# Performance work log

Measured on AMD Instinct MI355X. Metric: run time of the kernel, lower is better.

The kernel has to match this reference:

```python
import jax, jax.numpy as jnp
import numpy as np

B, GL, GF, N = 4, 4, 128, 1024
CS, CN, NA = 32, 16, 16
S, HS = 512, 512


def squash(s, axis):
    # mag_sq/(1+mag_sq) * s/mag == s * mag/(1+mag_sq)
    mag_sq = jnp.sum(s * s, axis=axis, keepdims=True)
    return s * (jnp.sqrt(mag_sq) / (1.0 + mag_sq))


def routing(u_hat, n_iter=3):
    # u_hat: [M, I, J, U]; dynamic routing, softmax over J, squash over J (as in source)
    M, I, J, U = u_hat.shape
    b = jnp.zeros((I, J), dtype=u_hat.dtype)
    v = None
    for _ in range(n_iter):
        c = jax.nn.softmax(b, axis=1)                       # [I, J]
        s = jnp.einsum('ij,miju->mju', c, u_hat)            # [M, J, U]
        v = squash(s, axis=1)                               # squash over J (torch dim=2)
        b = b + jnp.einsum('miju,mju->mij', u_hat, v).mean(axis=0)
    return v


def setup_inputs():
    key = jax.random.key(0)
    ks = jax.random.split(key, 7)
    sc = 0.1
    return {
        'graph_embed': jax.random.normal(ks[0], (B, GL, GF, N), jnp.float32),
        'hidden': jax.random.normal(ks[1], (B, S, HS), jnp.float32),
        'Wp': jax.random.normal(ks[2], (GL, CS, GL, GF), jnp.float32) * sc,  # per-unit conv kernels
        'bp': jax.random.normal(ks[3], (GL, CS), jnp.float32) * sc,
        'Wg': jax.random.normal(ks[4], (CS, CN, CS, GL), jnp.float32) * sc,  # graph caps [I,J,U,K]
        'Wa': jax.random.normal(ks[5], (CS + HS,), jnp.float32) * sc,        # attention_1 weight
        'Ws': jax.random.normal(ks[6], (CN, NA, CS, CS), jnp.float32) * sc,  # aspect caps [I,J,U,K]
    }


def _per_example(x, h, Wp, bp, Wg, Wa, Ws):
    # x: [GL, GF, N], h: [S, HS]
    gl, gf, n = x.shape
    # primary capsules: each unit's conv kernel covers all (GL,GF) -> full contraction
    u = jnp.einsum('uclf,lfn->ucn', Wp, x) + bp[:, :, None]   # [GL, CS, N]
    u = squash(u.reshape(gl, -1), axis=1)                     # squash over CS*N (torch dim=2)
    p = u.reshape(n, gl, CS)                                  # torch .view(-1, GL, CS)
    # graph capsule routing
    u_hat_g = jnp.einsum('ijuk,mik->miju', Wg, p.transpose(0, 2, 1))  # [N, CS, CN, CS]
    v_g = routing(u_hat_g)                                    # [N, CN, CS]
    g = v_g.reshape(n, CS, CN).mean(axis=0).reshape(CN, CS)   # torch .view semantics
    # adaptive attention: Linear([g;h]) with no bias, softmax over capsules
    score = jax.nn.softmax((g @ Wa[:CS])[None, :] + (h @ Wa[CS:])[:, None], axis=1)  # [S, CN]
    condensed = g[None, :, :] * score[:, :, None]             # [S, CN, CS]
    # aspect capsule routing (transpose(1,2) then layer-internal transpose cancel out)
    u_hat_a = jnp.einsum('ijuk,mik->miju', Ws, condensed)     # [S, CN, NA, CS]
    return routing(u_hat_a)                                   # [S, NA, CS]


def reference(graph_embed, hidden, Wp, bp, Wg, Wa, Ws):
    f = jax.vmap(_per_example, in_axes=(0, 0, None, None, None, None, None))
    return f(graph_embed, hidden, Wp, bp, Wg, Wa, Ws)   # [B, S, NA, CS]
```

## Files before the change

kernel.cpp:

```cpp
#include <hip/hip_runtime.h>
#include <math.h>


static constexpr int OFF_U  = 0;
static constexpr int OFF_S  = 524288;
static constexpr int OFF_SS = 2621440;
static constexpr int OFF_BG = 2621456;
static constexpr int OFF_G  = 2623504;
static constexpr int OFF_VA = 2625552;
static constexpr int OFF_MS = 2627600;
static constexpr int OFF_UH = 2758672;

__global__ void k_primary_part(const float* __restrict__ X, const float* __restrict__ Wp,
                               float* __restrict__ Upart)
{
    __shared__ float Wt[128 * 68];
    const int ct = blockIdx.x, nt = blockIdx.y;
    const int b = blockIdx.z >> 2, ks = blockIdx.z & 3;
    const int t = threadIdx.x;
    const int tn = t & 15, tc = t >> 4;
    const int c0 = ct * 64, n0 = nt * 64;
#pragma unroll
    for (int i = 0; i < 8; ++i) {
        const int idx = t + i * 256;
        const int c = idx >> 5, k4 = idx & 31;
        const float4 wv = *(const float4*)&Wp[(size_t)(c0 + c) * 512 + ks * 128 + k4 * 4];
        Wt[(k4 * 4 + 0) * 68 + c] = wv.x;
        Wt[(k4 * 4 + 1) * 68 + c] = wv.y;
        Wt[(k4 * 4 + 2) * 68 + c] = wv.z;
        Wt[(k4 * 4 + 3) * 68 + c] = wv.w;
    }
    __syncthreads();
    float acc[4][4] = {};
    const float* Xp = X + (size_t)b * 524288 + (size_t)(ks * 128) * 1024 + n0 + tn * 4;
#pragma unroll 4
    for (int k = 0; k < 128; ++k) {
        const float4 xv = *(const float4*)(Xp + (size_t)k * 1024);
        const float4 wv = *(const float4*)&Wt[k * 68 + tc * 4];
        const float w[4] = {wv.x, wv.y, wv.z, wv.w};
        const float x[4] = {xv.x, xv.y, xv.z, xv.w};
#pragma unroll
        for (int ci = 0; ci < 4; ++ci)
#pragma unroll
            for (int ni = 0; ni < 4; ++ni)
                acc[ci][ni] = fmaf(w[ci], x[ni], acc[ci][ni]);
    }
    float* up = Upart + (size_t)ks * 524288 + (size_t)b * 131072;
#pragma unroll
    for (int ci = 0; ci < 4; ++ci)
        *(float4*)&up[(size_t)(c0 + tc * 4 + ci) * 1024 + n0 + tn * 4] =
            make_float4(acc[ci][0], acc[ci][1], acc[ci][2], acc[ci][3]);
}

__global__ void k_reduceU(const float* __restrict__ Upart, const float* __restrict__ bp,
                          float* __restrict__ U, float* __restrict__ SS)
{
    __shared__ float red[256];
    const int blk = blockIdx.x, t = threadIdx.x;
    const int b = blk >> 5, cg = blk & 31;
    float ssq = 0.f;
#pragma unroll
    for (int i = 0; i < 4; ++i) {
        const int c = cg * 4 + i;
        const int f4 = b * 32768 + c * 256 + t;
        float4 s = ((const float4*)Upart)[f4];
#pragma unroll
        for (int ks = 1; ks < 4; ++ks) {
            const float4 p = ((const float4*)Upart)[ks * 131072 + f4];
            s.x += p.x; s.y += p.y; s.z += p.z; s.w += p.w;
        }
        const float bv = bp[c];
        s.x += bv; s.y += bv; s.z += bv; s.w += bv;
        ssq = fmaf(s.x, s.x, ssq); ssq = fmaf(s.y, s.y, ssq);
        ssq = fmaf(s.z, s.z, ssq); ssq = fmaf(s.w, s.w, ssq);
        ((float4*)U)[f4] = s;
    }
    red[t] = ssq;
    __syncthreads();
    for (int s = 128; s > 0; s >>= 1) {
        if (t < s) red[t] += red[t + s];
        __syncthreads();
    }
    if (t == 0) atomicAdd(&SS[b * 4 + (cg >> 3)], red[0]);
}

__global__ void k_smatmul(const float* __restrict__ U, const float* __restrict__ SS,
                          const float* __restrict__ Bg, const float* __restrict__ Wg,
                          float* __restrict__ S)
{
    __shared__ float Pt[64 * 65];
    __shared__ float Ct[64 * 65];
    __shared__ float cls[512];
    const int mt = blockIdx.x, jt = blockIdx.y, b = blockIdx.z;
    const int t = threadIdx.x;
    const int tj = t & 15, tm = t >> 4;
    if (t < 32) {
        float vals[16];
        float mx = -1e30f;
        for (int j = 0; j < 16; ++j) { vals[j] = Bg[b * 512 + t * 16 + j]; mx = fmaxf(mx, vals[j]); }
        float sum = 0.f;
        for (int j = 0; j < 16; ++j) { vals[j] = expf(vals[j] - mx); sum += vals[j]; }
        const float inv = 1.f / sum;
        for (int j = 0; j < 16; ++j) cls[t * 16 + j] = vals[j] * inv;
    }
    const float ss = SS[b * 4 + (mt >> 2)];
    const float sc = sqrtf(ss) / (1.f + ss);
    float acc[4][4] = {};
    const float* Ub = U + (size_t)b * 131072 + (size_t)mt * 64 * 128;
    __syncthreads();
    for (int kc = 0; kc < 2; ++kc) {
        for (int x = t; x < 64 * 64; x += 256) {
            const int r = x >> 6, cq = x & 63;
            Pt[r * 65 + cq] = Ub[r * 128 + kc * 64 + cq] * sc;
            const int q = kc * 64 + cq;
            const int i = q & 31, kk = q >> 5;
            const int ju = jt * 64 + r;
            const int j = ju >> 5, u = ju & 31;
            Ct[r * 65 + cq] = cls[i * 16 + j] * Wg[((i * 16 + j) * 32 + u) * 4 + kk];
        }
        __syncthreads();
        for (int q = 0; q < 64; ++q) {
            float pv[4], cv[4];
#pragma unroll
            for (int mm = 0; mm < 4; ++mm) pv[mm] = Pt[(tm * 4 + mm) * 65 + q];
#pragma unroll
            for (int jj = 0; jj < 4; ++jj) cv[jj] = Ct[(tj * 4 + jj) * 65 + q];
#pragma unroll
            for (int mm = 0; mm < 4; ++mm)
#pragma unroll
                for (int jj = 0; jj < 4; ++jj)
                    acc[mm][jj] = fmaf(pv[mm], cv[jj], acc[mm][jj]);
        }
        __syncthreads();
    }
#pragma unroll
    for (int mm = 0; mm < 4; ++mm) {
        float4 w = make_float4(acc[mm][0], acc[mm][1], acc[mm][2], acc[mm][3]);
        *(float4*)(S + (size_t)b * 524288 + (size_t)(mt * 64 + tm * 4 + mm) * 512
                     + jt * 64 + tj * 4) = w;
    }
}

__global__ void k_mag(const float* __restrict__ S, float* __restrict__ MS)
{
    const int t = threadIdx.x;
    const int u = t & 31, ml = t >> 5;
    const int m = blockIdx.x * 8 + ml;
    const int b = blockIdx.y;
    const float* row = S + (size_t)b * 524288 + (size_t)m * 512;
    float mag = 0.f;
#pragma unroll
    for (int j = 0; j < 16; ++j) { const float v = row[j * 32 + u]; mag = fmaf(v, v, mag); }
    MS[b * 32768 + m * 32 + u] = sqrtf(mag) / (1.f + mag);
}

__global__ void k_maggmean(const float* __restrict__ S, float* __restrict__ G)
{
    __shared__ float gacc[512];
    const int t = threadIdx.x;
    gacc[t] = 0.f; gacc[t + 256] = 0.f;
    const int u = t & 31, mlg = t >> 5;
    const int b = blockIdx.y;
    const int m0 = blockIdx.x * 32 + mlg * 4;
    float preg[16];
#pragma unroll
    for (int j = 0; j < 16; ++j) preg[j] = 0.f;
    __syncthreads();
#pragma unroll
    for (int mi = 0; mi < 4; ++mi) {
        const float* row = S + (size_t)b * 524288 + (size_t)(m0 + mi) * 512;
        float sv[16];
        float mag = 0.f;
#pragma unroll
        for (int j = 0; j < 16; ++j) { sv[j] = row[j * 32 + u]; mag = fmaf(sv[j], sv[j], mag); }
        const float msc = sqrtf(mag) / (1.f + mag);
#pragma unroll
        for (int j = 0; j < 16; ++j) preg[j] = fmaf(sv[j], msc, preg[j]);
    }
#pragma unroll
    for (int j = 0; j < 16; ++j) atomicAdd(&gacc[j * 32 + u], preg[j]);
    __syncthreads();
    atomicAdd(&G[b * 512 + t], gacc[t] * (1.f / 1024.f));
    atomicAdd(&G[b * 512 + 256 + t], gacc[t + 256] * (1.f / 1024.f));
}

__global__ void k_tbu(const float* __restrict__ U, const float* __restrict__ SS,
                      const float* __restrict__ S, const float* __restrict__ MS,
                      const float* __restrict__ Wg, float* __restrict__ Bg)
{
    __shared__ float Ps[64 * 132];
    __shared__ float Vs[64 * 68];
    __shared__ float bup[64];
    const int jt = blockIdx.x, mc = blockIdx.y, b = blockIdx.z;
    const int t = threadIdx.x;
    const int tq = t & 31, tjv = t >> 5;
    const int m0 = mc * 64;
    if (t < 64) bup[t] = 0.f;
    const float ss = SS[b * 4 + (mc >> 2)];
    const float sc = sqrtf(ss) / (1.f + ss);
#pragma unroll
    for (int i = 0; i < 8; ++i) {
        const int f4 = t + i * 256;
        const int r = f4 >> 5, q4 = f4 & 31;
        float4 v = *(const float4*)&U[(size_t)b * 131072 + (size_t)(m0 + r) * 128 + q4 * 4];
        v.x *= sc; v.y *= sc; v.z *= sc; v.w *= sc;
        *(float4*)&Ps[r * 132 + q4 * 4] = v;
    }
#pragma unroll
    for (int i = 0; i < 4; ++i) {
        const int f4 = t + i * 256;
        const int r = f4 >> 4, c4 = f4 & 15;
        const int m = m0 + r;
        float4 v = *(const float4*)&S[(size_t)b * 524288 + (size_t)m * 512 + jt * 64 + c4 * 4];
        const int ub = (c4 * 4) & 31;
        const float* msp = MS + b * 32768 + m * 32;
        v.x *= msp[ub + 0]; v.y *= msp[ub + 1]; v.z *= msp[ub + 2]; v.w *= msp[ub + 3];
        *(float4*)&Vs[r * 68 + c4 * 4] = v;
    }
    __syncthreads();
    float acc[4][8] = {};
#pragma unroll 2
    for (int m = 0; m < 64; ++m) {
        const float4 p4 = *(const float4*)&Ps[m * 132 + tq * 4];
        const float4 va = *(const float4*)&Vs[m * 68 + tjv * 8];
        const float4 vb = *(const float4*)&Vs[m * 68 + tjv * 8 + 4];
        const float pv[4] = {p4.x, p4.y, p4.z, p4.w};
        const float vv[8] = {va.x, va.y, va.z, va.w, vb.x, vb.y, vb.z, vb.w};
#pragma unroll
        for (int qi = 0; qi < 4; ++qi)
#pragma unroll
            for (int ji = 0; ji < 8; ++ji)
                acc[qi][ji] = fmaf(pv[qi], vv[ji], acc[qi][ji]);
    }
    const int k = tq >> 3;
    const int j_loc = tjv >> 2;
    const int j = jt * 2 + j_loc;
    const int u0 = (tjv & 3) * 8;
#pragma unroll
    for (int qi = 0; qi < 4; ++qi) {
        const int i = (tq & 7) * 4 + qi;
        const float* wp = Wg + ((i * 16 + j) * 32) * 4 + k;
        float s = 0.f;
#pragma unroll
        for (int ji = 0; ji < 8; ++ji)
            s = fmaf(wp[(u0 + ji) * 4], acc[qi][ji], s);
        s += __shfl_xor(s, 8);
        s += __shfl_xor(s, 16);
        s += __shfl_xor(s, 32);
        if ((t & 56) == 0) atomicAdd(&bup[i * 2 + j_loc], s);
    }
    __syncthreads();
    if (t < 64) {
        const int ii = t >> 1, jl = t & 1;
        atomicAdd(&Bg[b * 512 + ii * 16 + jt * 2 + jl], bup[t] * (1.f / 1024.f));
    }
}

__global__ void k_uhat(const float* __restrict__ G, const float* __restrict__ Wa,
                       const float* __restrict__ Ws, float* __restrict__ UH)
{
    const int b = blockIdx.y;
    const int t = threadIdx.x;
    __shared__ float g[512], cond[512], score[16], red[16];
    g[t] = G[b * 512 + t];
    g[t + 256] = G[b * 512 + 256 + t];
    __syncthreads();
    if (t < 16) {
        float s = 0.f;
        for (int u = 0; u < 32; ++u) s = fmaf(g[t * 32 + u], Wa[u], s);
        red[t] = s;
    }
    __syncthreads();
    if (t == 0) {
        float mx = -1e30f;
        for (int j = 0; j < 16; ++j) mx = fmaxf(mx, red[j]);
        float sum = 0.f;
        for (int j = 0; j < 16; ++j) { score[j] = expf(red[j] - mx); sum += score[j]; }
        const float inv = 1.f / sum;
        for (int j = 0; j < 16; ++j) score[j] *= inv;
    }
    __syncthreads();
    cond[t] = g[t] * score[t >> 5];
    cond[t + 256] = g[t + 256] * score[(t + 256) >> 5];
    __syncthreads();
    const int e0 = blockIdx.x * 1024 + t * 4;
    const int i = e0 >> 9;
    const float* cp = cond + i * 32;
    const float* wp = Ws + (size_t)e0 * 32;
    float res[4];
#pragma unroll
    for (int jj = 0; jj < 4; ++jj) {
        float s = 0.f;
#pragma unroll
        for (int k8 = 0; k8 < 8; ++k8) {
            const float4 w = *(const float4*)(wp + jj * 32 + k8 * 4);
            s = fmaf(w.x, cp[k8 * 4 + 0], s);
            s = fmaf(w.y, cp[k8 * 4 + 1], s);
            s = fmaf(w.z, cp[k8 * 4 + 2], s);
            s = fmaf(w.w, cp[k8 * 4 + 3], s);
        }
        res[jj] = s;
    }
    ((float4*)UH)[(b * 8192 + e0) >> 2] = make_float4(res[0], res[1], res[2], res[3]);
}

__global__ void k_route(const float* __restrict__ UH, float* __restrict__ VA)
{
    const int b = blockIdx.x;
    const int t = threadIdx.x;
    __shared__ float uh[8192], ba[256], cc[256], sbuf[512], msc[32];
#pragma unroll
    for (int i = 0; i < 8; ++i)
        ((float4*)uh)[i * 256 + t] = ((const float4*)UH)[b * 2048 + i * 256 + t];
    ba[t] = 0.f;
    __syncthreads();
    for (int it = 0; it < 3; ++it) {
        if (t < 16) {
            float mx = -1e30f;
            for (int j = 0; j < 16; ++j) mx = fmaxf(mx, ba[t * 16 + j]);
            float sum = 0.f;
            for (int j = 0; j < 16; ++j) { cc[t * 16 + j] = expf(ba[t * 16 + j] - mx); sum += cc[t * 16 + j]; }
            const float inv = 1.f / sum;
            for (int j = 0; j < 16; ++j) cc[t * 16 + j] *= inv;
        }
        __syncthreads();
        for (int h = 0; h < 2; ++h) {
            const int e = h * 256 + t;
            const int j = e >> 5;
            float s = 0.f;
            for (int i = 0; i < 16; ++i) s = fmaf(cc[i * 16 + j], uh[i * 512 + e], s);
            sbuf[e] = s;
        }
        __syncthreads();
        if (t < 32) {
            float mg = 0.f;
            for (int j = 0; j < 16; ++j) { const float x = sbuf[j * 32 + t]; mg = fmaf(x, x, mg); }
            msc[t] = sqrtf(mg) / (1.f + mg);
        }
        __syncthreads();
        for (int h = 0; h < 2; ++h) {
            const int e = h * 256 + t;
            sbuf[e] *= msc[e & 31];
        }
        __syncthreads();
        if (it < 2) {
            const int i = t >> 4, j = t & 15;
            float s = 0.f;
            for (int u = 0; u < 32; ++u) s = fmaf(uh[i * 512 + j * 32 + u], sbuf[j * 32 + u], s);
            ba[t] += s;
            __syncthreads();
        }
    }
    VA[b * 512 + t] = sbuf[t];
    VA[b * 512 + 256 + t] = sbuf[256 + t];
}

__global__ void k_out(const float* __restrict__ VA, float* __restrict__ out)
{
    const int idx = blockIdx.x * 256 + threadIdx.x;
    const int b = idx >> 16;
    const int jv4 = idx & 127;
    ((float4*)out)[idx] = ((const float4*)VA)[b * 128 + jv4];
}

extern "C" void kernel_launch(void* const* d_in, const int* in_sizes, int n_in,
                              void* d_out, int out_size, void* d_ws, size_t ws_size,
                              hipStream_t stream)
{
    const float* X   = (const float*)d_in[0];
    const float* Wp  = (const float*)d_in[2];
    const float* bp  = (const float*)d_in[3];
    const float* Wg  = (const float*)d_in[4];
    const float* Wa  = (const float*)d_in[5];
    const float* Wsp = (const float*)d_in[6];
    float* out = (float*)d_out;
    float* ws = (float*)d_ws;

    float* U  = ws + OFF_U;
    float* S  = ws + OFF_S;
    float* SS = ws + OFF_SS;
    float* Bg = ws + OFF_BG;
    float* G  = ws + OFF_G;
    float* VA = ws + OFF_VA;
    float* MS = ws + OFF_MS;
    float* UH = ws + OFF_UH;

    hipMemsetAsync(SS, 0, (16 + 2048 + 2048) * sizeof(float), stream);

    k_primary_part<<<dim3(2, 16, 16), 256, 0, stream>>>(X, Wp, S);
    k_reduceU<<<128, 256, 0, stream>>>(S, bp, U, SS);

    for (int it = 0; it < 3; ++it) {
        k_smatmul<<<dim3(16, 8, 4), 256, 0, stream>>>(U, SS, Bg, Wg, S);
        if (it < 2) {
            k_mag<<<dim3(128, 4), 256, 0, stream>>>(S, MS);
            k_tbu<<<dim3(8, 16, 4), 256, 0, stream>>>(U, SS, S, MS, Wg, Bg);
        } else {
            k_maggmean<<<dim3(32, 4), 256, 0, stream>>>(S, G);
        }
    }

    k_uhat<<<dim3(8, 4), 256, 0, stream>>>(G, Wa, Wsp, UH);
    k_route<<<4, 256, 0, stream>>>(UH, VA);
    k_out<<<1024, 256, 0, stream>>>(VA, out);
}
```

Measured before the change: 230.1 us.

## Fuse all stages into one persistent kernel with software grid barriers

Replaces the chain of about fourteen kernel launches and the memset with a single persistent kernel of 256 blocks that runs every stage in turn, separated by an atomic-counter grid barrier. Each stage's work is mapped onto the fixed block count with repeat loops. The aim is to remove launch gaps and per-kernel ramp-up and tail effects. In exchange, stages that used more blocks now run serially per block, many blocks sit idle in the small stages, and correctness depends on all 256 blocks being resident at once.

```diff
diff --git a/kernel.cpp b/kernel.cpp
--- a/kernel.cpp
+++ b/kernel.cpp
@@ -11,356 +11,412 @@
 static constexpr int OFF_MS = 2627600;
 static constexpr int OFF_UH = 2758672;
 
-__global__ void k_primary_part(const float* __restrict__ X, const float* __restrict__ Wp,
-                               float* __restrict__ Upart)
+#define NBLK 256
+
+__device__ unsigned g_cnt = 0;
+__device__ unsigned g_gen = 0;
+
+__device__ __forceinline__ void gbar()
 {
-    __shared__ float Wt[128 * 68];
-    const int ct = blockIdx.x, nt = blockIdx.y;
-    const int b = blockIdx.z >> 2, ks = blockIdx.z & 3;
+    __syncthreads();
+    if (threadIdx.x == 0) {
+        __threadfence();
+        const unsigned gen = atomicAdd(&g_gen, 0u);
+        if (atomicAdd(&g_cnt, 1u) == NBLK - 1u) {
+            atomicExch(&g_cnt, 0u);
+            __threadfence();
+            atomicAdd(&g_gen, 1u);
+        } else {
+            while (atomicAdd(&g_gen, 0u) == gen) { __builtin_amdgcn_s_sleep(8); }
+        }
+        __threadfence();
+    }
+    __syncthreads();
+}
+
+__global__ void __launch_bounds__(256, 1) k_mega(
+    const float* __restrict__ X,  const float* __restrict__ Wp,
+    const float* __restrict__ bp, const float* __restrict__ Wg,
+    const float* __restrict__ Wa, const float* __restrict__ Wsp,
+    float* __restrict__ ws, float* __restrict__ out)
+{
+    __shared__ float smem[12864];
+    const int bid = blockIdx.x;
     const int t = threadIdx.x;
-    const int tn = t & 15, tc = t >> 4;
-    const int c0 = ct * 64, n0 = nt * 64;
-#pragma unroll
-    for (int i = 0; i < 8; ++i) {
-        const int idx = t + i * 256;
-        const int c = idx >> 5, k4 = idx & 31;
-        const float4 wv = *(const float4*)&Wp[(size_t)(c0 + c) * 512 + ks * 128 + k4 * 4];
-        Wt[(k4 * 4 + 0) * 68 + c] = wv.x;
-        Wt[(k4 * 4 + 1) * 68 + c] = wv.y;
-        Wt[(k4 * 4 + 2) * 68 + c] = wv.z;
-        Wt[(k4 * 4 + 3) * 68 + c] = wv.w;
-    }
-    __syncthreads();
-    float acc[4][4] = {};
-    const float* Xp = X + (size_t)b * 524288 + (size_t)(ks * 128) * 1024 + n0 + tn * 4;
+
+    float* U  = ws + OFF_U;
+    float* S  = ws + OFF_S;
+    float* SS = ws + OFF_SS;
+    float* Bg = ws + OFF_BG;
+    float* G  = ws + OFF_G;
+    float* VA = ws + OFF_VA;
+    float* MS = ws + OFF_MS;
+    float* UH = ws + OFF_UH;
+
+    if (bid == 0) {
+        for (int i = t; i < 4112; i += 256) SS[i] = 0.f;
+    }
+
+    {
+        float* Wt = smem;
+        for (int rep = 0; rep < 2; ++rep) {
+            const int u = bid + rep * 256;
+            const int ct = u & 1, nt = (u >> 1) & 15;
+            const int z = u >> 5, b = z >> 2, ks = z & 3;
+            const int tn = t & 15, tc = t >> 4;
+            const int c0 = ct * 64, n0 = nt * 64;
+            __syncthreads();
+#pragma unroll
+            for (int i = 0; i < 8; ++i) {
+                const int idx = t + i * 256;
+                const int c = idx >> 5, k4 = idx & 31;
+                const float4 wv = *(const float4*)&Wp[(size_t)(c0 + c) * 512 + ks * 128 + k4 * 4];
+                Wt[(k4 * 4 + 0) * 68 + c] = wv.x;
+                Wt[(k4 * 4 + 1) * 68 + c] = wv.y;
+                Wt[(k4 * 4 + 2) * 68 + c] = wv.z;
+                Wt[(k4 * 4 + 3) * 68 + c] = wv.w;
+            }
+            __syncthreads();
+            float acc[4][4] = {};
+            const float* Xp = X + (size_t)b * 524288 + (size_t)(ks * 128) * 1024 + n0 + tn * 4;
 #pragma unroll 4
-    for (int k = 0; k < 128; ++k) {
-        const float4 xv = *(const float4*)(Xp + (size_t)k * 1024);
-        const float4 wv = *(const float4*)&Wt[k * 68 + tc * 4];
-        const float w[4] = {wv.x, wv.y, wv.z, wv.w};
-        const float x[4] = {xv.x, xv.y, xv.z, xv.w};
-#pragma unroll
-        for (int ci = 0; ci < 4; ++ci)
-#pragma unroll
-            for (int ni = 0; ni < 4; ++ni)
-                acc[ci][ni] = fmaf(w[ci], x[ni], acc[ci][ni]);
-    }
-    float* up = Upart + (size_t)ks * 524288 + (size_t)b * 131072;
-#pragma unroll
-    for (int ci = 0; ci < 4; ++ci)
-        *(float4*)&up[(size_t)(c0 + tc * 4 + ci) * 1024 + n0 + tn * 4] =
-            make_float4(acc[ci][0], acc[ci][1], acc[ci][2], acc[ci][3]);
-}
-
-__global__ void k_reduceU(const float* __restrict__ Upart, const float* __restrict__ bp,
-                          float* __restrict__ U, float* __restrict__ SS)
-{
-    __shared__ float red[256];
-    const int blk = blockIdx.x, t = threadIdx.x;
-    const int b = blk >> 5, cg = blk & 31;
-    float ssq = 0.f;
+            for (int k = 0; k < 128; ++k) {
+                const float4 xv = *(const float4*)(Xp + (size_t)k * 1024);
+                const float4 wv = *(const float4*)&Wt[k * 68 + tc * 4];
+                const float w[4] = {wv.x, wv.y, wv.z, wv.w};
+                const float x[4] = {xv.x, xv.y, xv.z, xv.w};
+#pragma unroll
+                for (int ci = 0; ci < 4; ++ci)
+#pragma unroll
+                    for (int ni = 0; ni < 4; ++ni)
+                        acc[ci][ni] = fmaf(w[ci], x[ni], acc[ci][ni]);
+            }
+            float* up = S + (size_t)ks * 524288 + (size_t)b * 131072;
+#pragma unroll
+            for (int ci = 0; ci < 4; ++ci)
+                *(float4*)&up[(size_t)(c0 + tc * 4 + ci) * 1024 + n0 + tn * 4] =
+                    make_float4(acc[ci][0], acc[ci][1], acc[ci][2], acc[ci][3]);
+        }
+    }
+    gbar();
+
+    if (bid < 128) {
+        float* red = smem;
+        const int b = bid >> 5, cg = bid & 31;
+        float ssq = 0.f;
+#pragma unroll
+        for (int i = 0; i < 4; ++i) {
+            const int c = cg * 4 + i;
+            const int f4 = b * 32768 + c * 256 + t;
+            float4 s = ((const float4*)S)[f4];
+#pragma unroll
+            for (int ks = 1; ks < 4; ++ks) {
+                const float4 p = ((const float4*)S)[ks * 131072 + f4];
+                s.x += p.x; s.y += p.y; s.z += p.z; s.w += p.w;
+            }
+            const float bv = bp[c];
+            s.x += bv; s.y += bv; s.z += bv; s.w += bv;
+            ssq = fmaf(s.x, s.x, ssq); ssq = fmaf(s.y, s.y, ssq);
+            ssq = fmaf(s.z, s.z, ssq); ssq = fmaf(s.w, s.w, ssq);
+            ((float4*)U)[f4] = s;
+        }
+        red[t] = ssq;
+        __syncthreads();
+        for (int s = 128; s > 0; s >>= 1) {
+            if (t < s) red[t] += red[t + s];
+            __syncthreads();
+        }
+        if (t == 0) atomicAdd(&SS[b * 4 + (cg >> 3)], red[0]);
+    }
+    gbar();
+
+    for (int it = 0; it < 3; ++it) {
+        {
+            float* Pt  = smem;
+            float* Ct  = smem + 4160;
+            float* cls = smem + 8320;
+            for (int rep = 0; rep < 2; ++rep) {
+                const int u = bid + rep * 256;
+                const int mt = u & 15, jt = (u >> 4) & 7, b = u >> 7;
+                const int tj = t & 15, tm = t >> 4;
+                __syncthreads();
+                if (t < 32) {
+                    float vals[16];
+                    float mx = -1e30f;
+                    for (int j = 0; j < 16; ++j) { vals[j] = Bg[b * 512 + t * 16 + j]; mx = fmaxf(mx, vals[j]); }
+                    float sum = 0.f;
+                    for (int j = 0; j < 16; ++j) { vals[j] = expf(vals[j] - mx); sum += vals[j]; }
+                    const float inv = 1.f / sum;
+                    for (int j = 0; j < 16; ++j) cls[t * 16 + j] = vals[j] * inv;
+                }
+                const float ssv = SS[b * 4 + (mt >> 2)];
+                const float sc = sqrtf(ssv) / (1.f + ssv);
+                float acc[4][4] = {};
+                const float* Ub = U + (size_t)b * 131072 + (size_t)mt * 64 * 128;
+                __syncthreads();
+                for (int kc = 0; kc < 2; ++kc) {
+                    for (int x = t; x < 64 * 64; x += 256) {
+                        const int r = x >> 6, cq = x & 63;
+                        Pt[r * 65 + cq] = Ub[r * 128 + kc * 64 + cq] * sc;
+                        const int q = kc * 64 + cq;
+                        const int i = q & 31, kk = q >> 5;
+                        const int ju = jt * 64 + r;
+                        const int j = ju >> 5, uu = ju & 31;
+                        Ct[r * 65 + cq] = cls[i * 16 + j] * Wg[((i * 16 + j) * 32 + uu) * 4 + kk];
+                    }
+                    __syncthreads();
+                    for (int q = 0; q < 64; ++q) {
+                        float pv[4], cv[4];
+#pragma unroll
+                        for (int mm = 0; mm < 4; ++mm) pv[mm] = Pt[(tm * 4 + mm) * 65 + q];
+#pragma unroll
+                        for (int jj = 0; jj < 4; ++jj) cv[jj] = Ct[(tj * 4 + jj) * 65 + q];
+#pragma unroll
+                        for (int mm = 0; mm < 4; ++mm)
+#pragma unroll
+                            for (int jj = 0; jj < 4; ++jj)
+                                acc[mm][jj] = fmaf(pv[mm], cv[jj], acc[mm][jj]);
+                    }
+                    __syncthreads();
+                }
+#pragma unroll
+                for (int mm = 0; mm < 4; ++mm) {
+                    float4 w = make_float4(acc[mm][0], acc[mm][1], acc[mm][2], acc[mm][3]);
+                    *(float4*)(S + (size_t)b * 524288 + (size_t)(mt * 64 + tm * 4 + mm) * 512
+                                 + jt * 64 + tj * 4) = w;
+                }
+            }
+        }
+        gbar();
+
+        if (it < 2) {
+            for (int rep = 0; rep < 2; ++rep) {
+                const int u = bid + rep * 256;
+                const int b = u >> 7, mg = u & 127;
+                const int uu = t & 31, ml = t >> 5;
+                const int m = mg * 8 + ml;
+                const float* row = S + (size_t)b * 524288 + (size_t)m * 512;
+                float mag = 0.f;
+#pragma unroll
+                for (int j = 0; j < 16; ++j) { const float v = row[j * 32 + uu]; mag = fmaf(v, v, mag); }
+                MS[b * 32768 + m * 32 + uu] = sqrtf(mag) / (1.f + mag);
+            }
+            gbar();
+
+            {
+                float* Ps  = smem;
+                float* Vs  = smem + 8448;
+                float* bup = smem + 12800;
+                for (int rep = 0; rep < 2; ++rep) {
+                    const int u = bid + rep * 256;
+                    const int jt = u & 7, mc = (u >> 3) & 15, b = u >> 7;
+                    const int tq = t & 31, tjv = t >> 5;
+                    const int m0 = mc * 64;
+                    __syncthreads();
+                    if (t < 64) bup[t] = 0.f;
+                    const float ssv = SS[b * 4 + (mc >> 2)];
+                    const float sc = sqrtf(ssv) / (1.f + ssv);
+#pragma unroll
+                    for (int i = 0; i < 8; ++i) {
+                        const int f4 = t + i * 256;
+                        const int r = f4 >> 5, q4 = f4 & 31;
+                        float4 v = *(const float4*)&U[(size_t)b * 131072 + (size_t)(m0 + r) * 128 + q4 * 4];
+                        v.x *= sc; v.y *= sc; v.z *= sc; v.w *= sc;
+                        *(float4*)&Ps[r * 132 + q4 * 4] = v;
+                    }
+#pragma unroll
+                    for (int i = 0; i < 4; ++i) {
+                        const int f4 = t + i * 256;
+                        const int r = f4 >> 4, c4 = f4 & 15;
+                        const int m = m0 + r;
+                        float4 v = *(const float4*)&S[(size_t)b * 524288 + (size_t)m * 512 + jt * 64 + c4 * 4];
+                        const int ub = (c4 * 4) & 31;
+                        const float* msp = MS + b * 32768 + m * 32;
+                        v.x *= msp[ub + 0]; v.y *= msp[ub + 1]; v.z *= msp[ub + 2]; v.w *= msp[ub + 3];
+                        *(float4*)&Vs[r * 68 + c4 * 4] = v;
+                    }
+                    __syncthreads();
+                    float acc[4][8] = {};
+#pragma unroll 2
+                    for (int m = 0; m < 64; ++m) {
+                        const float4 p4 = *(const float4*)&Ps[m * 132 + tq * 4];
+                        const float4 va = *(const float4*)&Vs[m * 68 + tjv * 8];
+                        const float4 vb = *(const float4*)&Vs[m * 68 + tjv * 8 + 4];
+                        const float pv[4] = {p4.x, p4.y, p4.z, p4.w};
+                        const float vv[8] = {va.x, va.y, va.z, va.w, vb.x, vb.y, vb.z, vb.w};
+#pragma unroll
+                        for (int qi = 0; qi < 4; ++qi)
+#pragma unroll
+                            for (int ji = 0; ji < 8; ++ji)
+                                acc[qi][ji] = fmaf(pv[qi], vv[ji], acc[qi][ji]);
+                    }
+                    const int k = tq >> 3;
+                    const int j_loc = tjv >> 2;
+                    const int j = jt * 2 + j_loc;
+                    const int u0 = (tjv & 3) * 8;
+#pragma unroll
+                    for (int qi = 0; qi < 4; ++qi) {
+                        const int i = (tq & 7) * 4 + qi;
+                        const float* wp = Wg + ((i * 16 + j) * 32) * 4 + k;
+                        float s = 0.f;
+#pragma unroll
+                        for (int ji = 0; ji < 8; ++ji)
+                            s = fmaf(wp[(u0 + ji) * 4], acc[qi][ji], s);
+                        s += __shfl_xor(s, 8);
+                        s += __shfl_xor(s, 16);
+                        s += __shfl_xor(s, 32);
+                        if ((t & 56) == 0) atomicAdd(&bup[i * 2 + j_loc], s);
+                    }
+                    __syncthreads();
+                    if (t < 64) {
+                        const int ii = t >> 1, jl = t & 1;
+                        atomicAdd(&Bg[b * 512 + ii * 16 + jt * 2 + jl], bup[t] * (1.f / 1024.f));
+                    }
+                }
+            }
+            gbar();
+        } else {
+            if (bid < 128) {
+                float* gacc = smem;
+                const int mt = bid & 31, b = bid >> 5;
+                gacc[t] = 0.f; gacc[t + 256] = 0.f;
+                const int uu = t & 31, mlg = t >> 5;
+                const int m0 = mt * 32 + mlg * 4;
+                float preg[16];
+#pragma unroll
+                for (int j = 0; j < 16; ++j) preg[j] = 0.f;
+                __syncthreads();
+#pragma unroll
+                for (int mi = 0; mi < 4; ++mi) {
+                    const float* row = S + (size_t)b * 524288 + (size_t)(m0 + mi) * 512;
+                    float sv[16];
+                    float mag = 0.f;
+#pragma unroll
+                    for (int j = 0; j < 16; ++j) { sv[j] = row[j * 32 + uu]; mag = fmaf(sv[j], sv[j], mag); }
+                    const float msc = sqrtf(mag) / (1.f + mag);
+#pragma unroll
+                    for (int j = 0; j < 16; ++j) preg[j] = fmaf(sv[j], msc, preg[j]);
+                }
+#pragma unroll
+                for (int j = 0; j < 16; ++j) atomicAdd(&gacc[j * 32 + uu], preg[j]);
+                __syncthreads();
+                atomicAdd(&G[b * 512 + t], gacc[t] * (1.f / 1024.f));
+                atomicAdd(&G[b * 512 + 256 + t], gacc[t + 256] * (1.f / 1024.f));
+            }
+            gbar();
+        }
+    }
+
+    if (bid < 32) {
+        float* g     = smem;
+        float* cond  = smem + 512;
+        float* score = smem + 1024;
+        float* red   = smem + 1040;
+        const int slice = bid & 7, b = bid >> 3;
+        g[t] = G[b * 512 + t];
+        g[t + 256] = G[b * 512 + 256 + t];
+        __syncthreads();
+        if (t < 16) {
+            float s = 0.f;
+            for (int uu = 0; uu < 32; ++uu) s = fmaf(g[t * 32 + uu], Wa[uu], s);
+            red[t] = s;
+        }
+        __syncthreads();
+        if (t == 0) {
+            float mx = -1e30f;
+            for (int j = 0; j < 16; ++j) mx = fmaxf(mx, red[j]);
+            float sum = 0.f;
+            for (int j = 0; j < 16; ++j) { score[j] = expf(red[j] - mx); sum += score[j]; }
+            const float inv = 1.f / sum;
+            for (int j = 0; j < 16; ++j) score[j] *= inv;
+        }
+        __syncthreads();
+        cond[t] = g[t] * score[t >> 5];
+        cond[t + 256] = g[t + 256] * score[(t + 256) >> 5];
+        __syncthreads();
+        const int e0 = slice * 1024 + t * 4;
+        const int i = e0 >> 9;
+        const float* cp = cond + i * 32;
+        const float* wp = Wsp + (size_t)e0 * 32;
+        float res[4];
+#pragma unroll
+        for (int jj = 0; jj < 4; ++jj) {
+            float s = 0.f;
+#pragma unroll
+            for (int k8 = 0; k8 < 8; ++k8) {
+                const float4 w = *(const float4*)(wp + jj * 32 + k8 * 4);
+                s = fmaf(w.x, cp[k8 * 4 + 0], s);
+                s = fmaf(w.y, cp[k8 * 4 + 1], s);
+                s = fmaf(w.z, cp[k8 * 4 + 2], s);
+                s = fmaf(w.w, cp[k8 * 4 + 3], s);
+            }
+            res[jj] = s;
+        }
+        ((float4*)UH)[(b * 8192 + e0) >> 2] = make_float4(res[0], res[1], res[2], res[3]);
+    }
+    gbar();
+
+    if (bid < 4) {
+        float* uh   = smem;
+        float* ba   = smem + 8192;
+        float* cc   = smem + 8448;
+        float* sbuf = smem + 8704;
+        float* msc  = smem + 9216;
+        const int b = bid;
+#pragma unroll
+        for (int i = 0; i < 8; ++i)
+            ((float4*)uh)[i * 256 + t] = ((const float4*)UH)[b * 2048 + i * 256 + t];
+        ba[t] = 0.f;
+        __syncthreads();
+        for (int it = 0; it < 3; ++it) {
+            if (t < 16) {
+                float mx = -1e30f;
+                for (int j = 0; j < 16; ++j) mx = fmaxf(mx, ba[t * 16 + j]);
+                float sum = 0.f;
+                for (int j = 0; j < 16; ++j) { cc[t * 16 + j] = expf(ba[t * 16 + j] - mx); sum += cc[t * 16 + j]; }
+                const float inv = 1.f / sum;
+                for (int j = 0; j < 16; ++j) cc[t * 16 + j] *= inv;
+            }
+            __syncthreads();
+            for (int h = 0; h < 2; ++h) {
+                const int e = h * 256 + t;
+                const int j = e >> 5;
+                float s = 0.f;
+                for (int i = 0; i < 16; ++i) s = fmaf(cc[i * 16 + j], uh[i * 512 + e], s);
+                sbuf[e] = s;
+            }
+            __syncthreads();
+            if (t < 32) {
+                float mg = 0.f;
+                for (int j = 0; j < 16; ++j) { const float x = sbuf[j * 32 + t]; mg = fmaf(x, x, mg); }
+                msc[t] = sqrtf(mg) / (1.f + mg);
+            }
+            __syncthreads();
+            for (int h = 0; h < 2; ++h) {
+                const int e = h * 256 + t;
+                sbuf[e] *= msc[e & 31];
+            }
+            __syncthreads();
+            if (it < 2) {
+                const int i = t >> 4, j = t & 15;
+                float s = 0.f;
+                for (int uu = 0; uu < 32; ++uu) s = fmaf(uh[i * 512 + j * 32 + uu], sbuf[j * 32 + uu], s);
+                ba[t] += s;
+                __syncthreads();
+            }
+        }
+        VA[b * 512 + t] = sbuf[t];
+        VA[b * 512 + 256 + t] = sbuf[256 + t];
+    }
+    gbar();
+
 #pragma unroll
     for (int i = 0; i < 4; ++i) {
-        const int c = cg * 4 + i;
-        const int f4 = b * 32768 + c * 256 + t;
-        float4 s = ((const float4*)Upart)[f4];
-#pragma unroll
-        for (int ks = 1; ks < 4; ++ks) {
-            const float4 p = ((const float4*)Upart)[ks * 131072 + f4];
-            s.x += p.x; s.y += p.y; s.z += p.z; s.w += p.w;
-        }
-        const float bv = bp[c];
-        s.x += bv; s.y += bv; s.z += bv; s.w += bv;
-        ssq = fmaf(s.x, s.x, ssq); ssq = fmaf(s.y, s.y, ssq);
-        ssq = fmaf(s.z, s.z, ssq); ssq = fmaf(s.w, s.w, ssq);
-        ((float4*)U)[f4] = s;
-    }
-    red[t] = ssq;
-    __syncthreads();
-    for (int s = 128; s > 0; s >>= 1) {
-        if (t < s) red[t] += red[t + s];
-        __syncthreads();
-    }
-    if (t == 0) atomicAdd(&SS[b * 4 + (cg >> 3)], red[0]);
-}
-
-__global__ void k_smatmul(const float* __restrict__ U, const float* __restrict__ SS,
-                          const float* __restrict__ Bg, const float* __restrict__ Wg,
-                          float* __restrict__ S)
-{
-    __shared__ float Pt[64 * 65];
-    __shared__ float Ct[64 * 65];
-    __shared__ float cls[512];
-    const int mt = blockIdx.x, jt = blockIdx.y, b = blockIdx.z;
-    const int t = threadIdx.x;
-    const int tj = t & 15, tm = t >> 4;
-    if (t < 32) {
-        float vals[16];
-        float mx = -1e30f;
-        for (int j = 0; j < 16; ++j) { vals[j] = Bg[b * 512 + t * 16 + j]; mx = fmaxf(mx, vals[j]); }
-        float sum = 0.f;
-        for (int j = 0; j < 16; ++j) { vals[j] = expf(vals[j] - mx); sum += vals[j]; }
-        const float inv = 1.f / sum;
-        for (int j = 0; j < 16; ++j) cls[t * 16 + j] = vals[j] * inv;
-    }
-    const float ss = SS[b * 4 + (mt >> 2)];
-    const float sc = sqrtf(ss) / (1.f + ss);
-    float acc[4][4] = {};
-    const float* Ub = U + (size_t)b * 131072 + (size_t)mt * 64 * 128;
-    __syncthreads();
-    for (int kc = 0; kc < 2; ++kc) {
-        for (int x = t; x < 64 * 64; x += 256) {
-            const int r = x >> 6, cq = x & 63;
-            Pt[r * 65 + cq] = Ub[r * 128 + kc * 64 + cq] * sc;
-            const int q = kc * 64 + cq;
-            const int i = q & 31, kk = q >> 5;
-            const int ju = jt * 64 + r;
-            const int j = ju >> 5, u = ju & 31;
-            Ct[r * 65 + cq] = cls[i * 16 + j] * Wg[((i * 16 + j) * 32 + u) * 4 + kk];
-        }
-        __syncthreads();
-        for (int q = 0; q < 64; ++q) {
-            float pv[4], cv[4];
-#pragma unroll
-            for (int mm = 0; mm < 4; ++mm) pv[mm] = Pt[(tm * 4 + mm) * 65 + q];
-#pragma unroll
-            for (int jj = 0; jj < 4; ++jj) cv[jj] = Ct[(tj * 4 + jj) * 65 + q];
-#pragma unroll
-            for (int mm = 0; mm < 4; ++mm)
-#pragma unroll
-                for (int jj = 0; jj < 4; ++jj)
-                    acc[mm][jj] = fmaf(pv[mm], cv[jj], acc[mm][jj]);
-        }
-        __syncthreads();
-    }
-#pragma unroll
-    for (int mm = 0; mm < 4; ++mm) {
-        float4 w = make_float4(acc[mm][0], acc[mm][1], acc[mm][2], acc[mm][3]);
-        *(float4*)(S + (size_t)b * 524288 + (size_t)(mt * 64 + tm * 4 + mm) * 512
-                     + jt * 64 + tj * 4) = w;
-    }
-}
-
-__global__ void k_mag(const float* __restrict__ S, float* __restrict__ MS)
-{
-    const int t = threadIdx.x;
-    const int u = t & 31, ml = t >> 5;
-    const int m = blockIdx.x * 8 + ml;
-    const int b = blockIdx.y;
-    const float* row = S + (size_t)b * 524288 + (size_t)m * 512;
-    float mag = 0.f;
-#pragma unroll
-    for (int j = 0; j < 16; ++j) { const float v = row[j * 32 + u]; mag = fmaf(v, v, mag); }
-    MS[b * 32768 + m * 32 + u] = sqrtf(mag) / (1.f + mag);
-}
-
-__global__ void k_maggmean(const float* __restrict__ S, float* __restrict__ G)
-{
-    __shared__ float gacc[512];
-    const int t = threadIdx.x;
-    gacc[t] = 0.f; gacc[t + 256] = 0.f;
-    const int u = t & 31, mlg = t >> 5;
-    const int b = blockIdx.y;
-    const int m0 = blockIdx.x * 32 + mlg * 4;
-    float preg[16];
-#pragma unroll
-    for (int j = 0; j < 16; ++j) preg[j] = 0.f;
-    __syncthreads();
-#pragma unroll
-    for (int mi = 0; mi < 4; ++mi) {
-        const float* row = S + (size_t)b * 524288 + (size_t)(m0 + mi) * 512;
-        float sv[16];
-        float mag = 0.f;
-#pragma unroll
-        for (int j = 0; j < 16; ++j) { sv[j] = row[j * 32 + u]; mag = fmaf(sv[j], sv[j], mag); }
-        const float msc = sqrtf(mag) / (1.f + mag);
-#pragma unroll
-        for (int j = 0; j < 16; ++j) preg[j] = fmaf(sv[j], msc, preg[j]);
-    }
-#pragma unroll
-    for (int j = 0; j < 16; ++j) atomicAdd(&gacc[j * 32 + u], preg[j]);
-    __syncthreads();
-    atomicAdd(&G[b * 512 + t], gacc[t] * (1.f / 1024.f));
-    atomicAdd(&G[b * 512 + 256 + t], gacc[t + 256] * (1.f / 1024.f));
-}
-
-__global__ void k_tbu(const float* __restrict__ U, const float* __restrict__ SS,
-                      const float* __restrict__ S, const float* __restrict__ MS,
-                      const float* __restrict__ Wg, float* __restrict__ Bg)
-{
-    __shared__ float Ps[64 * 132];
-    __shared__ float Vs[64 * 68];
-    __shared__ float bup[64];
-    const int jt = blockIdx.x, mc = blockIdx.y, b = blockIdx.z;
-    const int t = threadIdx.x;
-    const int tq = t & 31, tjv = t >> 5;
-    const int m0 = mc * 64;
-    if (t < 64) bup[t] = 0.f;
-    const float ss = SS[b * 4 + (mc >> 2)];
-    const float sc = sqrtf(ss) / (1.f + ss);
-#pragma unroll
-    for (int i = 0; i < 8; ++i) {
-        const int f4 = t + i * 256;
-        const int r = f4 >> 5, q4 = f4 & 31;
-        float4 v = *(const float4*)&U[(size_t)b * 131072 + (size_t)(m0 + r) * 128 + q4 * 4];
-        v.x *= sc; v.y *= sc; v.z *= sc; v.w *= sc;
-        *(float4*)&Ps[r * 132 + q4 * 4] = v;
-    }
-#pragma unroll
-    for (int i = 0; i < 4; ++i) {
-        const int f4 = t + i * 256;
-        const int r = f4 >> 4, c4 = f4 & 15;
-        const int m = m0 + r;
-        float4 v = *(const float4*)&S[(size_t)b * 524288 + (size_t)m * 512 + jt * 64 + c4 * 4];
-        const int ub = (c4 * 4) & 31;
-        const float* msp = MS + b * 32768 + m * 32;
-        v.x *= msp[ub + 0]; v.y *= msp[ub + 1]; v.z *= msp[ub + 2]; v.w *= msp[ub + 3];
-        *(float4*)&Vs[r * 68 + c4 * 4] = v;
-    }
-    __syncthreads();
-    float acc[4][8] = {};
-#pragma unroll 2
-    for (int m = 0; m < 64; ++m) {
-        const float4 p4 = *(const float4*)&Ps[m * 132 + tq * 4];
-        const float4 va = *(const float4*)&Vs[m * 68 + tjv * 8];
-        const float4 vb = *(const float4*)&Vs[m * 68 + tjv * 8 + 4];
-        const float pv[4] = {p4.x, p4.y, p4.z, p4.w};
-        const float vv[8] = {va.x, va.y, va.z, va.w, vb.x, vb.y, vb.z, vb.w};
-#pragma unroll
-        for (int qi = 0; qi < 4; ++qi)
-#pragma unroll
-            for (int ji = 0; ji < 8; ++ji)
-                acc[qi][ji] = fmaf(pv[qi], vv[ji], acc[qi][ji]);
-    }
-    const int k = tq >> 3;
-    const int j_loc = tjv >> 2;
-    const int j = jt * 2 + j_loc;
-    const int u0 = (tjv & 3) * 8;
-#pragma unroll
-    for (int qi = 0; qi < 4; ++qi) {
-        const int i = (tq & 7) * 4 + qi;
-        const float* wp = Wg + ((i * 16 + j) * 32) * 4 + k;
-        float s = 0.f;
-#pragma unroll
-        for (int ji = 0; ji < 8; ++ji)
-            s = fmaf(wp[(u0 + ji) * 4], acc[qi][ji], s);
-        s += __shfl_xor(s, 8);
-        s += __shfl_xor(s, 16);
-        s += __shfl_xor(s, 32);
-        if ((t & 56) == 0) atomicAdd(&bup[i * 2 + j_loc], s);
-    }
-    __syncthreads();
-    if (t < 64) {
-        const int ii = t >> 1, jl = t & 1;
-        atomicAdd(&Bg[b * 512 + ii * 16 + jt * 2 + jl], bup[t] * (1.f / 1024.f));
-    }
-}
-
-__global__ void k_uhat(const float* __restrict__ G, const float* __restrict__ Wa,
-                       const float* __restrict__ Ws, float* __restrict__ UH)
-{
-    const int b = blockIdx.y;
-    const int t = threadIdx.x;
-    __shared__ float g[512], cond[512], score[16], red[16];
-    g[t] = G[b * 512 + t];
-    g[t + 256] = G[b * 512 + 256 + t];
-    __syncthreads();
-    if (t < 16) {
-        float s = 0.f;
-        for (int u = 0; u < 32; ++u) s = fmaf(g[t * 32 + u], Wa[u], s);
-        red[t] = s;
-    }
-    __syncthreads();
-    if (t == 0) {
-        float mx = -1e30f;
-        for (int j = 0; j < 16; ++j) mx = fmaxf(mx, red[j]);
-        float sum = 0.f;
-        for (int j = 0; j < 16; ++j) { score[j] = expf(red[j] - mx); sum += score[j]; }
-        const float inv = 1.f / sum;
-        for (int j = 0; j < 16; ++j) score[j] *= inv;
-    }
-    __syncthreads();
-    cond[t] = g[t] * score[t >> 5];
-    cond[t + 256] = g[t + 256] * score[(t + 256) >> 5];
-    __syncthreads();
-    const int e0 = blockIdx.x * 1024 + t * 4;
-    const int i = e0 >> 9;
-    const float* cp = cond + i * 32;
-    const float* wp = Ws + (size_t)e0 * 32;
-    float res[4];
-#pragma unroll
-    for (int jj = 0; jj < 4; ++jj) {
-        float s = 0.f;
-#pragma unroll
-        for (int k8 = 0; k8 < 8; ++k8) {
-            const float4 w = *(const float4*)(wp + jj * 32 + k8 * 4);
-            s = fmaf(w.x, cp[k8 * 4 + 0], s);
-            s = fmaf(w.y, cp[k8 * 4 + 1], s);
-            s = fmaf(w.z, cp[k8 * 4 + 2], s);
-            s = fmaf(w.w, cp[k8 * 4 + 3], s);
-        }
-        res[jj] = s;
-    }
-    ((float4*)UH)[(b * 8192 + e0) >> 2] = make_float4(res[0], res[1], res[2], res[3]);
-}
-
-__global__ void k_route(const float* __restrict__ UH, float* __restrict__ VA)
-{
-    const int b = blockIdx.x;
-    const int t = threadIdx.x;
-    __shared__ float uh[8192], ba[256], cc[256], sbuf[512], msc[32];
-#pragma unroll
-    for (int i = 0; i < 8; ++i)
-        ((float4*)uh)[i * 256 + t] = ((const float4*)UH)[b * 2048 + i * 256 + t];
-    ba[t] = 0.f;
-    __syncthreads();
-    for (int it = 0; it < 3; ++it) {
-        if (t < 16) {
-            float mx = -1e30f;
-            for (int j = 0; j < 16; ++j) mx = fmaxf(mx, ba[t * 16 + j]);
-            float sum = 0.f;
-            for (int j = 0; j < 16; ++j) { cc[t * 16 + j] = expf(ba[t * 16 + j] - mx); sum += cc[t * 16 + j]; }
-            const float inv = 1.f / sum;
-            for (int j = 0; j < 16; ++j) cc[t * 16 + j] *= inv;
-        }
-        __syncthreads();
-        for (int h = 0; h < 2; ++h) {
-            const int e = h * 256 + t;
-            const int j = e >> 5;
-            float s = 0.f;
-            for (int i = 0; i < 16; ++i) s = fmaf(cc[i * 16 + j], uh[i * 512 + e], s);
-            sbuf[e] = s;
-        }
-        __syncthreads();
-        if (t < 32) {
-            float mg = 0.f;
-            for (int j = 0; j < 16; ++j) { const float x = sbuf[j * 32 + t]; mg = fmaf(x, x, mg); }
-            msc[t] = sqrtf(mg) / (1.f + mg);
-        }
-        __syncthreads();
-        for (int h = 0; h < 2; ++h) {
-            const int e = h * 256 + t;
-            sbuf[e] *= msc[e & 31];
-        }
-        __syncthreads();
-        if (it < 2) {
-            const int i = t >> 4, j = t & 15;
-            float s = 0.f;
-            for (int u = 0; u < 32; ++u) s = fmaf(uh[i * 512 + j * 32 + u], sbuf[j * 32 + u], s);
-            ba[t] += s;
-            __syncthreads();
-        }
-    }
-    VA[b * 512 + t] = sbuf[t];
-    VA[b * 512 + 256 + t] = sbuf[256 + t];
-}
-
-__global__ void k_out(const float* __restrict__ VA, float* __restrict__ out)
-{
-    const int idx = blockIdx.x * 256 + threadIdx.x;
-    const int b = idx >> 16;
-    const int jv4 = idx & 127;
-    ((float4*)out)[idx] = ((const float4*)VA)[b * 128 + jv4];
+        const int idx = bid * 1024 + i * 256 + t;
+        const int b = idx >> 16;
+        const int jv4 = idx & 127;
+        ((float4*)out)[idx] = ((const float4*)VA)[b * 128 + jv4];
+    }
 }
 
 extern "C" void kernel_launch(void* const* d_in, const int* in_sizes, int n_in,
@@ -374,33 +430,7 @@
     const float* Wa  = (const float*)d_in[5];
     const float* Wsp = (const float*)d_in[6];
     float* out = (float*)d_out;
-    float* ws = (float*)d_ws;
-
-    float* U  = ws + OFF_U;
-    float* S  = ws + OFF_S;
-    float* SS = ws + OFF_SS;
-    float* Bg = ws + OFF_BG;
-    float* G  = ws + OFF_G;
-    float* VA = ws + OFF_VA;
-    float* MS = ws + OFF_MS;
-    float* UH = ws + OFF_UH;
-
-    hipMemsetAsync(SS, 0, (16 + 2048 + 2048) * sizeof(float), stream);
-
-    k_primary_part<<<dim3(2, 16, 16), 256, 0, stream>>>(X, Wp, S);
-    k_reduceU<<<128, 256, 0, stream>>>(S, bp, U, SS);
-
-    for (int it = 0; it < 3; ++it) {
-        k_smatmul<<<dim3(16, 8, 4), 256, 0, stream>>>(U, SS, Bg, Wg, S);
-        if (it < 2) {
-            k_mag<<<dim3(128, 4), 256, 0, stream>>>(S, MS);
-            k_tbu<<<dim3(8, 16, 4), 256, 0, stream>>>(U, SS, S, MS, Wg, Bg);
-        } else {
-            k_maggmean<<<dim3(32, 4), 256, 0, stream>>>(S, G);
-        }
-    }
-
-    k_uhat<<<dim3(8, 4), 256, 0, stream>>>(G, Wa, Wsp, UH);
-    k_route<<<4, 256, 0, stream>>>(UH, VA);
-    k_out<<<1024, 256, 0, stream>>>(VA, out);
+    float* ws  = (float*)d_ws;
+
+    k_mega<<<dim3(NBLK), dim3(256), 0, stream>>>(X, Wp, bp, Wg, Wa, Wsp, ws, out);
 }
```

Result: slower. 580.0 us (+152.0%).
